# Performance work log

Measured on AMD Instinct MI355X. Metric: run time of the kernel, lower is better.

## Reference

```python
import jax, jax.numpy as jnp
import numpy as np

K_EPSILON = 1e-4  # matches pytorch3d norm_weighted_sum kEpsilon


def setup_inputs() -> dict:
    key = jax.random.key(0)
    k1, k2, k3 = jax.random.split(key, 3)
    N, K, H, W = 4, 8, 256, 256
    C, P = 64, 100000
    fragments = jax.random.randint(k1, (N, K, H, W), 0, P, dtype=jnp.int64)
    alphas = jax.random.uniform(k2, (N, K, H, W), dtype=jnp.float32)
    ptclds = jax.random.normal(k3, (C, P), dtype=jnp.float32)
    return {"fragments": fragments, "alphas": alphas, "ptclds": ptclds}


def reference(fragments, alphas, ptclds):
    # fragments: (N,K,H,W) int point indices, -1 = empty pixel slot
    # alphas:    (N,K,H,W) float weights
    # ptclds:    (C,P) packed point features
    mask = fragments >= 0                                   # (N,K,H,W)
    safe_idx = jnp.where(mask, fragments, 0)
    w = jnp.where(mask, alphas, 0.0)                        # zero invalid slots
    feats = ptclds[:, safe_idx]                             # (C,N,K,H,W) gather
    num = jnp.einsum('cnkhw,nkhw->nchw', feats, w)          # weighted sum over K
    denom = jnp.maximum(w.sum(axis=1), K_EPSILON)           # (N,H,W)
    return num / denom[:, None, :, :]                       # (N,C,H,W)
```

## Files before the change

### kernel.cpp

```cpp
#include <hip/hip_runtime.h>
#include <hip/hip_fp16.h>

#define K_EPSILON 0.0001f

constexpr int N = 4, K = 8, H = 256, W = 256, C = 64;
constexpr int NSLICE = 4, SC = 16;

__global__ __launch_bounds__(256) void transpose_slices2(
    const float* __restrict__ src, __half2* __restrict__ dst, int P, int PB) {
  __shared__ float tile[16][260];
  const int t = threadIdx.x;
  const int s = blockIdx.x / PB;
  const int p0 = (blockIdx.x - s * PB) * 256;

  #pragma unroll
  for (int i = 0; i < 16; ++i) {
    int c = s * SC + i;
    int p = p0 + t;
    tile[i][t] = (p < P) ? src[(size_t)c * P + p] : 0.0f;
  }
  __syncthreads();

  const int j = t & 7;
  const int pp0 = t >> 3;
  #pragma unroll
  for (int i = 0; i < 8; ++i) {
    int pp = pp0 + i * 32;
    int p = p0 + pp;
    if (p < P)
      dst[((size_t)s * P + p) * 8 + j] =
          __floats2half2_rn(tile[2 * j][pp], tile[2 * j + 1][pp]);
  }
}

__global__ __launch_bounds__(256) void compositor_fused(
    const int* __restrict__ frag, const float* __restrict__ alpha,
    const __half2* __restrict__ table, float* __restrict__ out, int P) {
  __shared__ uint32_t s_pk[256][9];
  __shared__ float    s_out[256][SC + 1];
  const int t = threadIdx.x;
  const int B = blockIdx.x;
  const int slice = (B & 7) >> 1;
  const int rowid = ((B >> 3) << 1) | (B & 1);
  const int n = rowid >> 8, h = rowid & 255;

  {
    float a[K];
    int id[K];
    float den = 0.0f;
    #pragma unroll
    for (int k = 0; k < K; ++k) {
      size_t g = (((size_t)(n * K + k)) << 16) + ((size_t)h << 8) + t;
      int idx = frag[g];
      float av = alpha[g];
      bool m = idx >= 0;
      id[k] = m ? idx : 0;
      a[k] = m ? av : 0.0f;
      den += a[k];
    }
    float inv = 1.0f / fmaxf(den, K_EPSILON);
    #pragma unroll
    for (int k = 0; k < K; ++k) {
      uint32_t wq = (uint32_t)rintf(a[k] * inv * 32767.0f);
      s_pk[t][k] = (wq << 17) | (uint32_t)id[k];
    }
  }
  __syncthreads();

  const __half2* tab = table + (size_t)slice * P * 8;
  const int lane = t & 63, wid = t >> 6;
  const int pg = lane >> 3, j = lane & 7;
  const float invq = 1.0f / 32767.0f;

  #pragma unroll
  for (int iter = 0; iter < 8; ++iter) {
    int pix = iter * 32 + wid * 8 + pg;
    float acc0 = 0.0f, acc1 = 0.0f;
    #pragma unroll
    for (int k = 0; k < K; ++k) {
      uint32_t v = s_pk[pix][k];
      int idx = (int)(v & 0x1FFFF);
      float w = (float)(v >> 17) * invq;
      float2 f = __half22float2(tab[(size_t)idx * 8 + j]);
      acc0 += w * f.x;
      acc1 += w * f.y;
    }
    s_out[pix][2 * j]     = acc0;
    s_out[pix][2 * j + 1] = acc1;
  }
  __syncthreads();

  #pragma unroll
  for (int i = 0; i < SC; ++i) {
    int c = slice * SC + i;
    out[(((size_t)(n * C + c)) << 16) + ((size_t)h << 8) + t] = s_out[t][i];
  }
}

__global__ __launch_bounds__(256) void compositor_fallback(
    const int* __restrict__ frag, const float* __restrict__ alpha,
    const float* __restrict__ pt, float* __restrict__ out, int P) {
  __shared__ int   s_idx[K][64];
  __shared__ float s_a[K][64];
  __shared__ float s_out[64][67];

  const int t = threadIdx.x;
  const int tile = blockIdx.x;
  const int w0 = (tile & 3) * 64;
  const int h = (tile >> 2) & (H - 1);
  const int n = tile >> 10;

  #pragma unroll
  for (int i = 0; i < 2; ++i) {
    int f = t + i * 256;
    int k = f >> 6, wo = f & 63;
    size_t g = (((size_t)(n * K + k) * H + h) * W) + w0 + wo;
    s_idx[k][wo] = frag[g];
    s_a[k][wo]   = alpha[g];
  }
  __syncthreads();

  const int lane = t & 63;
  const int wid  = t >> 6;
  for (int jj = 0; jj < 16; ++jj) {
    int pix = wid * 16 + jj;
    float acc = 0.0f, den = 0.0f;
    #pragma unroll
    for (int k = 0; k < K; ++k) {
      int idx = s_idx[k][pix];
      float a = s_a[k][pix];
      if (idx < 0) a = 0.0f;
      int safe = idx < 0 ? 0 : idx;
      acc += a * pt[(size_t)lane * P + safe];
      den += a;
    }
    s_out[pix][lane] = acc / fmaxf(den, K_EPSILON);
  }
  __syncthreads();

  #pragma unroll
  for (int i = 0; i < 16; ++i) {
    int c = (t >> 6) + i * 4;
    int wo = t & 63;
    size_t g = (((size_t)(n * C + c) * H + h) * W) + w0 + wo;
    out[g] = s_out[wo][c];
  }
}

extern "C" void kernel_launch(void* const* d_in, const int* in_sizes, int n_in,
                              void* d_out, int out_size, void* d_ws, size_t ws_size,
                              hipStream_t stream) {
  const int*   frag   = (const int*)d_in[0];
  const float* alpha  = (const float*)d_in[1];
  const float* ptclds = (const float*)d_in[2];
  float*       out    = (float*)d_out;

  const int P = in_sizes[2] / C;
  const size_t tableBytes = (size_t)P * C * sizeof(__half);

  if (ws_size >= tableBytes) {
    __half2* ptT = (__half2*)d_ws;
    const int PB = (P + 255) / 256;
    transpose_slices2<<<NSLICE * PB, 256, 0, stream>>>(ptclds, ptT, P, PB);
    compositor_fused<<<NSLICE * N * H, 256, 0, stream>>>(frag, alpha, ptT, out, P);
  } else {
    compositor_fallback<<<N * H * (W / 64), 256, 0, stream>>>(frag, alpha,
                                                              ptclds, out, P);
  }
}
```

Before: 64.35 us.

## Store point table as full-channel fp16 rows and gather 128-byte rows per pixel

The transposed point table now keeps all 64 fp16 channels of a point contiguous (128 bytes per point) instead of four 16-channel slices. Each compositor block handles 128 pixels across all channels, with eight lanes each doing a 16-byte vector load per sample. Fragment and alpha data are now read once per pixel rather than once per channel slice, and each random gather covers a full contiguous row. The cost is fewer blocks, more accumulator registers per thread, and half the threads idle during the weight-packing phase.

```diff
diff --git a/kernel.cpp b/kernel.cpp
--- a/kernel.cpp
+++ b/kernel.cpp
@@ -4,53 +4,53 @@
 #define K_EPSILON 0.0001f
 
 constexpr int N = 4, K = 8, H = 256, W = 256, C = 64;
-constexpr int NSLICE = 4, SC = 16;
 
-__global__ __launch_bounds__(256) void transpose_slices2(
+__global__ __launch_bounds__(256) void transpose_pt(
     const float* __restrict__ src, __half2* __restrict__ dst, int P, int PB) {
-  __shared__ float tile[16][260];
+  __shared__ float tile[32][257];
   const int t = threadIdx.x;
-  const int s = blockIdx.x / PB;
-  const int p0 = (blockIdx.x - s * PB) * 256;
+  const int cb = blockIdx.x / PB;
+  const int p0 = (blockIdx.x - cb * PB) * 256;
 
   #pragma unroll
-  for (int i = 0; i < 16; ++i) {
-    int c = s * SC + i;
+  for (int i = 0; i < 32; ++i) {
+    int c = cb * 32 + i;
     int p = p0 + t;
     tile[i][t] = (p < P) ? src[(size_t)c * P + p] : 0.0f;
   }
   __syncthreads();
 
-  const int j = t & 7;
-  const int pp0 = t >> 3;
+  const int jj = t & 15;
+  const int pl0 = t >> 4;
   #pragma unroll
-  for (int i = 0; i < 8; ++i) {
-    int pp = pp0 + i * 32;
-    int p = p0 + pp;
+  for (int i = 0; i < 16; ++i) {
+    int pl = pl0 + i * 16;
+    int p = p0 + pl;
     if (p < P)
-      dst[((size_t)s * P + p) * 8 + j] =
-          __floats2half2_rn(tile[2 * j][pp], tile[2 * j + 1][pp]);
+      dst[(size_t)p * 32 + cb * 16 + jj] =
+          __floats2half2_rn(tile[2 * jj][pl], tile[2 * jj + 1][pl]);
   }
 }
 
-__global__ __launch_bounds__(256) void compositor_fused(
+__global__ __launch_bounds__(256, 4) void compositor_wide(
     const int* __restrict__ frag, const float* __restrict__ alpha,
     const __half2* __restrict__ table, float* __restrict__ out, int P) {
-  __shared__ uint32_t s_pk[256][9];
-  __shared__ float    s_out[256][SC + 1];
+  __shared__ uint32_t s_pk[128][9];
+  __shared__ float    s_out[128][65];
+
   const int t = threadIdx.x;
   const int B = blockIdx.x;
-  const int slice = (B & 7) >> 1;
-  const int rowid = ((B >> 3) << 1) | (B & 1);
+  const int rowid = B >> 1;
   const int n = rowid >> 8, h = rowid & 255;
+  const int w0 = (B & 1) * 128;
 
-  {
+  if (t < 128) {
     float a[K];
     int id[K];
     float den = 0.0f;
     #pragma unroll
     for (int k = 0; k < K; ++k) {
-      size_t g = (((size_t)(n * K + k)) << 16) + ((size_t)h << 8) + t;
+      size_t g = (((size_t)(n * K + k)) << 16) + ((size_t)h << 8) + w0 + t;
       int idx = frag[g];
       float av = alpha[g];
       bool m = idx >= 0;
@@ -67,33 +67,45 @@
   }
   __syncthreads();
 
-  const __half2* tab = table + (size_t)slice * P * 8;
+  const char* tb = (const char*)table;
   const int lane = t & 63, wid = t >> 6;
-  const int pg = lane >> 3, j = lane & 7;
+  const int pg = lane >> 3;
+  const int j = lane & 3 ? (lane & 7) : (lane & 7);
+  const int jc = lane & 7;
   const float invq = 1.0f / 32767.0f;
 
   #pragma unroll
-  for (int iter = 0; iter < 8; ++iter) {
+  for (int iter = 0; iter < 4; ++iter) {
     int pix = iter * 32 + wid * 8 + pg;
-    float acc0 = 0.0f, acc1 = 0.0f;
+    float acc0 = 0.f, acc1 = 0.f, acc2 = 0.f, acc3 = 0.f;
+    float acc4 = 0.f, acc5 = 0.f, acc6 = 0.f, acc7 = 0.f;
     #pragma unroll
     for (int k = 0; k < K; ++k) {
       uint32_t v = s_pk[pix][k];
       int idx = (int)(v & 0x1FFFF);
       float w = (float)(v >> 17) * invq;
-      float2 f = __half22float2(tab[(size_t)idx * 8 + j]);
-      acc0 += w * f.x;
-      acc1 += w * f.y;
+      uint4 d = *(const uint4*)(tb + ((size_t)idx << 7) + (jc << 4));
+      float2 f0 = __half22float2(*(const __half2*)&d.x);
+      float2 f1 = __half22float2(*(const __half2*)&d.y);
+      float2 f2 = __half22float2(*(const __half2*)&d.z);
+      float2 f3 = __half22float2(*(const __half2*)&d.w);
+      acc0 += w * f0.x; acc1 += w * f0.y;
+      acc2 += w * f1.x; acc3 += w * f1.y;
+      acc4 += w * f2.x; acc5 += w * f2.y;
+      acc6 += w * f3.x; acc7 += w * f3.y;
     }
-    s_out[pix][2 * j]     = acc0;
-    s_out[pix][2 * j + 1] = acc1;
+    float* row = &s_out[pix][8 * jc];
+    row[0] = acc0; row[1] = acc1; row[2] = acc2; row[3] = acc3;
+    row[4] = acc4; row[5] = acc5; row[6] = acc6; row[7] = acc7;
   }
   __syncthreads();
 
+  const int w = t & 127, chalf = t >> 7;
   #pragma unroll
-  for (int i = 0; i < SC; ++i) {
-    int c = slice * SC + i;
-    out[(((size_t)(n * C + c)) << 16) + ((size_t)h << 8) + t] = s_out[t][i];
+  for (int i = 0; i < 32; ++i) {
+    int c = i * 2 + chalf;
+    out[(((size_t)(n * C + c)) << 16) + ((size_t)h << 8) + w0 + w] =
+        s_out[w][c];
   }
 }
 
@@ -161,8 +173,8 @@
   if (ws_size >= tableBytes) {
     __half2* ptT = (__half2*)d_ws;
     const int PB = (P + 255) / 256;
-    transpose_slices2<<<NSLICE * PB, 256, 0, stream>>>(ptclds, ptT, P, PB);
-    compositor_fused<<<NSLICE * N * H, 256, 0, stream>>>(frag, alpha, ptT, out, P);
+    transpose_pt<<<2 * PB, 256, 0, stream>>>(ptclds, ptT, P, PB);
+    compositor_wide<<<2 * N * H, 256, 0, stream>>>(frag, alpha, ptT, out, P);
   } else {
     compositor_fallback<<<N * H * (W / 64), 256, 0, stream>>>(frag, alpha,
                                                               ptclds, out, P);
```

Result: faster. 57.78 us (-10.2%).

## Quantize point features to per-point int8 and gather 16-byte channel slices

Applied to the files above, without the earlier changes.

Replaces the fp16 transposed table with a per-point symmetric int8 table plus a float scale array, split into two 32-channel slices. Each thread now gathers a 16-byte vector holding 16 channels per neighbor, and the scale and offset are folded into the per-pixel weights. The aim is to halve the gathered table bytes and the number of gather instructions. In exchange the features lose precision to 8 bits per point, which may exceed tolerance.

```diff
diff --git a/kernel.cpp b/kernel.cpp
--- a/kernel.cpp
+++ b/kernel.cpp
@@ -4,53 +4,80 @@
 #define K_EPSILON 0.0001f
 
 constexpr int N = 4, K = 8, H = 256, W = 256, C = 64;
-constexpr int NSLICE = 4, SC = 16;
-
-__global__ __launch_bounds__(256) void transpose_slices2(
-    const float* __restrict__ src, __half2* __restrict__ dst, int P, int PB) {
-  __shared__ float tile[16][260];
+
+__global__ __launch_bounds__(256) void quantize_pt(
+    const float* __restrict__ src, uint8_t* __restrict__ table,
+    float* __restrict__ scale, int P) {
+  __shared__ float tile[64][129];
+  __shared__ float s_inv[128];
   const int t = threadIdx.x;
-  const int s = blockIdx.x / PB;
-  const int p0 = (blockIdx.x - s * PB) * 256;
-
-  #pragma unroll
-  for (int i = 0; i < 16; ++i) {
-    int c = s * SC + i;
+  const int p0 = blockIdx.x * 128;
+  const int pl = t & 127, ch2 = t >> 7;
+
+  #pragma unroll
+  for (int i = 0; i < 32; ++i) {
+    int c = i * 2 + ch2;
+    int p = p0 + pl;
+    tile[c][pl] = (p < P) ? src[(size_t)c * P + p] : 0.0f;
+  }
+  __syncthreads();
+
+  if (t < 128) {
+    float m = 1e-9f;
+    #pragma unroll
+    for (int c = 0; c < 64; ++c) m = fmaxf(m, fabsf(tile[c][t]));
     int p = p0 + t;
-    tile[i][t] = (p < P) ? src[(size_t)c * P + p] : 0.0f;
-  }
-  __syncthreads();
-
-  const int j = t & 7;
-  const int pp0 = t >> 3;
-  #pragma unroll
-  for (int i = 0; i < 8; ++i) {
-    int pp = pp0 + i * 32;
-    int p = p0 + pp;
-    if (p < P)
-      dst[((size_t)s * P + p) * 8 + j] =
-          __floats2half2_rn(tile[2 * j][pp], tile[2 * j + 1][pp]);
-  }
-}
-
-__global__ __launch_bounds__(256) void compositor_fused(
+    if (p < P) scale[p] = m / 127.0f;
+    s_inv[t] = 127.0f / m;
+  }
+  __syncthreads();
+
+  const int pw = t >> 1, jc = t & 1;
+  const int p = p0 + pw;
+  if (p < P) {
+    float inv = s_inv[pw];
+    #pragma unroll
+    for (int s = 0; s < 2; ++s) {
+      uint32_t wv[4];
+      #pragma unroll
+      for (int q = 0; q < 4; ++q) {
+        uint32_t b = 0;
+        #pragma unroll
+        for (int b4 = 0; b4 < 4; ++b4) {
+          int c = s * 32 + jc * 16 + q * 4 + b4;
+          int u = (int)rintf(tile[c][pw] * inv) + 128;
+          b |= ((uint32_t)(u & 255)) << (8 * b4);
+        }
+        wv[q] = b;
+      }
+      *(uint4*)&table[((size_t)s * P + p) * 32 + jc * 16] =
+          make_uint4(wv[0], wv[1], wv[2], wv[3]);
+    }
+  }
+}
+
+__global__ __launch_bounds__(256) void compositor_resident(
     const int* __restrict__ frag, const float* __restrict__ alpha,
-    const __half2* __restrict__ table, float* __restrict__ out, int P) {
-  __shared__ uint32_t s_pk[256][9];
-  __shared__ float    s_out[256][SC + 1];
+    const uint8_t* __restrict__ table, const float* __restrict__ scale,
+    float* __restrict__ out, int P) {
+  __shared__ uint32_t s_idx[128][9];
+  __shared__ float    s_ws[128][11];
+  __shared__ float    s_out[128][33];
   const int t = threadIdx.x;
   const int B = blockIdx.x;
-  const int slice = (B & 7) >> 1;
-  const int rowid = ((B >> 3) << 1) | (B & 1);
-  const int n = rowid >> 8, h = rowid & 255;
-
-  {
+  const int slice = (B & 7) >> 2;
+  const int rid = ((B >> 3) << 2) | (B & 3);
+  const int row = rid >> 1;
+  const int n = row >> 8, h = row & 255;
+  const int w0 = (rid & 1) * 128;
+
+  if (t < 128) {
     float a[K];
     int id[K];
     float den = 0.0f;
     #pragma unroll
     for (int k = 0; k < K; ++k) {
-      size_t g = (((size_t)(n * K + k)) << 16) + ((size_t)h << 8) + t;
+      size_t g = (((size_t)(n * K + k)) << 16) + ((size_t)h << 8) + w0 + t;
       int idx = frag[g];
       float av = alpha[g];
       bool m = idx >= 0;
@@ -59,41 +86,57 @@
       den += a[k];
     }
     float inv = 1.0f / fmaxf(den, K_EPSILON);
+    float bias = 0.0f;
     #pragma unroll
     for (int k = 0; k < K; ++k) {
-      uint32_t wq = (uint32_t)rintf(a[k] * inv * 32767.0f);
-      s_pk[t][k] = (wq << 17) | (uint32_t)id[k];
-    }
-  }
-  __syncthreads();
-
-  const __half2* tab = table + (size_t)slice * P * 8;
+      float ws = a[k] * inv * scale[id[k]];
+      s_ws[t][k] = ws;
+      s_idx[t][k] = (uint32_t)id[k];
+      bias += ws;
+    }
+    s_ws[t][8] = 128.0f * bias;
+  }
+  __syncthreads();
+
+  const uint8_t* tab = table + (size_t)slice * P * 32;
   const int lane = t & 63, wid = t >> 6;
-  const int pg = lane >> 3, j = lane & 7;
-  const float invq = 1.0f / 32767.0f;
-
-  #pragma unroll
-  for (int iter = 0; iter < 8; ++iter) {
-    int pix = iter * 32 + wid * 8 + pg;
-    float acc0 = 0.0f, acc1 = 0.0f;
-    #pragma unroll
-    for (int k = 0; k < K; ++k) {
-      uint32_t v = s_pk[pix][k];
-      int idx = (int)(v & 0x1FFFF);
-      float w = (float)(v >> 17) * invq;
-      float2 f = __half22float2(tab[(size_t)idx * 8 + j]);
-      acc0 += w * f.x;
-      acc1 += w * f.y;
-    }
-    s_out[pix][2 * j]     = acc0;
-    s_out[pix][2 * j + 1] = acc1;
-  }
-  __syncthreads();
-
-  #pragma unroll
-  for (int i = 0; i < SC; ++i) {
-    int c = slice * SC + i;
-    out[(((size_t)(n * C + c)) << 16) + ((size_t)h << 8) + t] = s_out[t][i];
+  const int pg = lane >> 1, jc = lane & 1;
+  const int pix = wid * 32 + pg;
+
+  float acc[16];
+  {
+    float bias = s_ws[pix][8];
+    #pragma unroll
+    for (int i = 0; i < 16; ++i) acc[i] = -bias;
+  }
+  #pragma unroll
+  for (int k = 0; k < K; ++k) {
+    uint32_t idx = s_idx[pix][k];
+    float ws = s_ws[pix][k];
+    uint4 d = *(const uint4*)(tab + ((size_t)idx << 5) + (jc << 4));
+    uint32_t wd[4] = {d.x, d.y, d.z, d.w};
+    #pragma unroll
+    for (int q = 0; q < 4; ++q) {
+      #pragma unroll
+      for (int b = 0; b < 4; ++b) {
+        acc[q * 4 + b] += ws * (float)((wd[q] >> (8 * b)) & 255u);
+      }
+    }
+  }
+  {
+    float* row_out = &s_out[pix][jc * 16];
+    #pragma unroll
+    for (int i = 0; i < 16; ++i) row_out[i] = acc[i];
+  }
+  __syncthreads();
+
+  const int w = t & 127, half = t >> 7;
+  const size_t base = ((size_t)h << 8) + w0 + w;
+  #pragma unroll
+  for (int ii = 0; ii < 16; ++ii) {
+    int i = half * 16 + ii;
+    int c = slice * 32 + i;
+    out[(((size_t)(n * C + c)) << 16) + base] = s_out[w][i];
   }
 }
 
@@ -156,13 +199,15 @@
   float*       out    = (float*)d_out;
 
   const int P = in_sizes[2] / C;
-  const size_t tableBytes = (size_t)P * C * sizeof(__half);
-
-  if (ws_size >= tableBytes) {
-    __half2* ptT = (__half2*)d_ws;
-    const int PB = (P + 255) / 256;
-    transpose_slices2<<<NSLICE * PB, 256, 0, stream>>>(ptclds, ptT, P, PB);
-    compositor_fused<<<NSLICE * N * H, 256, 0, stream>>>(frag, alpha, ptT, out, P);
+  const size_t tableBytes = (size_t)P * C;
+  const size_t scaleBytes = (size_t)P * sizeof(float);
+
+  if (ws_size >= tableBytes + scaleBytes) {
+    uint8_t* tab = (uint8_t*)d_ws;
+    float*   sc  = (float*)((char*)d_ws + tableBytes);
+    quantize_pt<<<(P + 127) / 128, 256, 0, stream>>>(ptclds, tab, sc, P);
+    compositor_resident<<<2 * 2 * N * H, 256, 0, stream>>>(frag, alpha, tab,
+                                                           sc, out, P);
   } else {
     compositor_fallback<<<N * H * (W / 64), 256, 0, stream>>>(frag, alpha,
                                                               ptclds, out, P);
```

New measurement: 66.32 us. 3.1% more time.
